# Kernel tuning notes

Measured on AMD Instinct MI355X. Metric: run time of the kernel, lower is better.

Reference implementation:

```python
import jax, jax.numpy as jnp
import numpy as np
from jax import lax

HEADS = 8
LN_EPS = 1e-5


def setup_inputs() -> dict:
    key = jax.random.key(0)
    k = jax.random.split(key, 8)
    B, C, H, W, r = 4, 64, 64, 64, 4
    T = H * W
    x = jax.random.normal(k[0], (B, C, H, W), dtype=jnp.float32)
    conv_w = jax.random.normal(k[1], (C, C, r, r), dtype=jnp.float32) * 0.02  # OIHW
    conv_b = jnp.zeros((C,), dtype=jnp.float32)
    ln_g = jnp.ones((C,), dtype=jnp.float32)
    ln_b = jnp.zeros((C,), dtype=jnp.float32)
    Wqkv = jax.random.normal(k[2], (C, 3 * C), dtype=jnp.float32) * 0.02  # to_qvk (no bias)
    W0 = jax.random.normal(k[3], (C, C), dtype=jnp.float32) * 0.02  # output proj (no bias)
    E = jax.random.normal(k[4], (T, T // 4), dtype=jnp.float32)  # Linformer proj (randn in torch fwd)
    return {"x": x, "conv_w": conv_w, "conv_b": conv_b, "ln_g": ln_g,
            "ln_b": ln_b, "Wqkv": Wqkv, "W0": W0, "E": E}


def _layernorm2d(y, g, b):
    # LayerNorm over channel dim of NCHW (torch: permute to NHWC, LN last dim)
    yt = y.transpose(0, 2, 3, 1)  # b h w c
    mu = yt.mean(-1, keepdims=True)
    var = ((yt - mu) ** 2).mean(-1, keepdims=True)
    yt = (yt - mu) * lax.rsqrt(var + LN_EPS) * g + b
    return yt.transpose(0, 3, 1, 2)


def reference(x, conv_w, conv_b, ln_g, ln_b, Wqkv, W0, E):
    B, C, H, W = x.shape
    T = H * W
    dh = C // HEADS
    r = conv_w.shape[-1]

    # reducer: conv(stride=r) + LayerNorm2d. NOTE: faithful to the torch module,
    # this result is computed but NEVER used by the output (dead code in source).
    red = lax.conv_general_dilated(x, conv_w, (r, r), 'VALID',
                                   dimension_numbers=('NCHW', 'OIHW', 'NCHW'))
    red = red + conv_b[None, :, None, None]
    _red = _layernorm2d(red, ln_g, ln_b)  # unused, matches source

    # tokens from full-resolution x: b c h w -> b (h w) c
    xf = x.reshape(B, C, T).transpose(0, 2, 1)  # [B,T,C]
    qkv = xf @ Wqkv  # [B,T,3C]
    # rearrange 'b t (d k h)' with k=3, h=HEADS -> composite order (d, k, h)
    qkv = qkv.reshape(B, T, dh, 3, HEADS)
    q = qkv[:, :, :, 0, :].transpose(0, 3, 1, 2)  # [B,h,T,d]
    kk = qkv[:, :, :, 1, :].transpose(0, 3, 1, 2)
    v = qkv[:, :, :, 2, :].transpose(0, 3, 1, 2)

    # Linformer low-rank projection of V and K: [B,h,T,d] x [T,k] -> [B,h,k,d]
    v = jnp.einsum('bhjd,jk->bhkd', v, E)
    kk = jnp.einsum('bhjd,jk->bhkd', kk, E)

    scale = dh ** -0.5
    scores = jnp.einsum('bhid,bhjd->bhij', q, kk) * scale  # [B,h,T,k]
    attn = jax.nn.softmax(scores, axis=-1)
    out = jnp.einsum('bhij,bhjd->bhid', attn, v)  # [B,h,T,d]

    out = out.transpose(0, 2, 1, 3).reshape(B, T, C)  # b h i d -> b i (h d)
    out = out @ W0  # [B,T,C]
    return out.transpose(0, 2, 1).reshape(B, C, H, W)
```

## Files before the change

### kernel.cpp

```cpp
#include <hip/hip_runtime.h>

#define T_DIM 4096
#define KD    1024
#define SCALE 0.35355339059327373f

typedef __attribute__((ext_vector_type(8))) short bf16x8;
typedef __attribute__((ext_vector_type(4))) short bf16x4;
typedef __attribute__((ext_vector_type(4))) float f32x4;

__device__ inline unsigned short f2bf(float f) {
  unsigned u = __float_as_uint(f);
  unsigned r = u + 0x7fffu + ((u >> 16) & 1u);
  return (unsigned short)(r >> 16);
}

__device__ inline unsigned cvt_pk_bf16(float a, float b) {
  unsigned ua = __float_as_uint(a); ua += 0x7fffu + ((ua >> 16) & 1u);
  unsigned ub = __float_as_uint(b); ub += 0x7fffu + ((ub >> 16) & 1u);
  return (ua >> 16) | (ub & 0xffff0000u);
}

__device__ inline unsigned pk_trunc(float a, float b) {
  return (__float_as_uint(a) >> 16) | (__float_as_uint(b) & 0xffff0000u);
}

__device__ inline bf16x4 mk4(unsigned lo, unsigned hi) {
  union { unsigned u[2]; bf16x4 v; } x; x.u[0] = lo; x.u[1] = hi; return x.v;
}

__device__ inline bf16x8 mk8(unsigned a, unsigned b, unsigned c, unsigned d) {
  union { unsigned u[4]; bf16x8 v; } x;
  x.u[0] = a; x.u[1] = b; x.u[2] = c; x.u[3] = d; return x.v;
}

__device__ inline f32x4 mfma16(bf16x4 a, bf16x4 b, f32x4 c) {
  bf16x8 a8 = {}, b8 = {};
  a8[0] = a[0]; a8[1] = a[1]; a8[2] = a[2]; a8[3] = a[3];
  b8[0] = b[0]; b8[1] = b[1]; b8[2] = b[2]; b8[3] = b[3];
  return __builtin_amdgcn_mfma_f32_16x16x32_bf16(a8, b8, c, 0, 0, 0);
}

__global__ __launch_bounds__(256) void k_front(const float* __restrict__ x,
                                               const float* __restrict__ E,
                                               const float* __restrict__ Wqkv,
                                               float* __restrict__ partial,
                                               float* __restrict__ Q,
                                               float* __restrict__ out) {
  const int bid = blockIdx.x;
  const int tid = threadIdx.x;

  ((float4*)out)[(size_t)bid * 256 + tid] = make_float4(0.f, 0.f, 0.f, 0.f);

  if (bid < 512) {
    const int kb = bid & 7;
    const int b  = (bid >> 3) & 3;
    const int s  = bid >> 5;
    const int k0 = kb * 128;
    const int lane = tid & 63;
    const int w = tid >> 6;
    const int li = lane & 15, lg = lane >> 4;

    f32x4 acc[4][2] = {};
#pragma unroll 2
    for (int tb = 0; tb < 8; ++tb) {
      const int tbase = s * 256 + tb * 32 + lg * 8;
      bf16x8 bq[2];
#pragma unroll
      for (int nt = 0; nt < 2; ++nt) {
        const int kcol = k0 + w * 32 + nt * 16 + li;
        float bv[8];
#pragma unroll
        for (int j = 0; j < 8; ++j)
          bv[j] = E[(size_t)(tbase + j) * KD + kcol];
        bq[nt] = mk8(cvt_pk_bf16(bv[0], bv[1]), cvt_pk_bf16(bv[2], bv[3]),
                     cvt_pk_bf16(bv[4], bv[5]), cvt_pk_bf16(bv[6], bv[7]));
      }
#pragma unroll
      for (int mt = 0; mt < 4; ++mt) {
        const float* ap = x + ((size_t)b * 64 + mt * 16 + li) * T_DIM + tbase;
        float4 a0 = *(const float4*)(ap);
        float4 a1 = *(const float4*)(ap + 4);
        bf16x8 af8 = mk8(cvt_pk_bf16(a0.x, a0.y), cvt_pk_bf16(a0.z, a0.w),
                         cvt_pk_bf16(a1.x, a1.y), cvt_pk_bf16(a1.z, a1.w));
        acc[mt][0] = __builtin_amdgcn_mfma_f32_16x16x32_bf16(af8, bq[0], acc[mt][0], 0, 0, 0);
        acc[mt][1] = __builtin_amdgcn_mfma_f32_16x16x32_bf16(af8, bq[1], acc[mt][1], 0, 0, 0);
      }
    }
    float* pb = partial + ((size_t)s * 4 + b) * (64 * KD);
#pragma unroll
    for (int mt = 0; mt < 4; ++mt)
#pragma unroll
      for (int nt = 0; nt < 2; ++nt) {
        const int row = mt * 16 + lg * 4;
        const int col = k0 + w * 32 + nt * 16 + li;
#pragma unroll
        for (int reg = 0; reg < 4; ++reg)
          pb[(size_t)(row + reg) * KD + col] = acc[mt][nt][reg];
      }
  } else {
    const int idx = bid - 512;
    const int g  = idx & 7;
    const int tt = (idx >> 3) & 15;
    const int b  = idx >> 7;
    const int t  = tt * 256 + tid;
    const int col0 = g * 24;

    float acc[8];
#pragma unroll
    for (int j = 0; j < 8; ++j) acc[j] = 0.f;
    const float* xb = x + (size_t)b * 64 * T_DIM + t;
#pragma unroll 4
    for (int c = 0; c < 64; ++c) {
      float xv = xb[(size_t)c * T_DIM];
      const float* wr = Wqkv + c * 192 + col0;
#pragma unroll
      for (int h = 0; h < 8; ++h) acc[h] += xv * wr[h];
    }
#pragma unroll
    for (int h = 0; h < 8; ++h)
      Q[(((size_t)(b * 8 + h)) * 8 + g) * T_DIM + t] = acc[h];
  }
}

__global__ __launch_bounds__(256) void k_xkv(const float* __restrict__ partial,
                                             const float* __restrict__ Wqkv,
                                             uint2* __restrict__ Kg,
                                             unsigned short* __restrict__ Vg) {
  __shared__ unsigned short XPs[64 * 72];
  const int kb = blockIdx.x;
  const int h  = blockIdx.y;
  const int b  = blockIdx.z;
  const int tid = threadIdx.x;

  {
    const int kk = tid & 63;
    const int cg = tid >> 6;
#pragma unroll
    for (int u = 0; u < 16; ++u) {
      const int c = cg * 16 + u;
      const size_t src = (size_t)c * KD + kb * 64 + kk;
      float a = 0.f;
#pragma unroll
      for (int s = 0; s < 16; ++s)
        a += partial[((size_t)s * 4 + b) * (64 * KD) + src];
      XPs[c * 72 + kk] = f2bf(a);
    }
  }
  __syncthreads();

  const int klocal = tid & 63;
  const int sel    = (tid >> 6) & 1;
  const int dg     = tid >> 7;
  const int k      = kb * 64 + klocal;

  float acc[4];
#pragma unroll
  for (int d = 0; d < 4; ++d) acc[d] = 0.f;
#pragma unroll 4
  for (int c = 0; c < 64; ++c) {
    float xv = __uint_as_float((unsigned)XPs[c * 72 + klocal] << 16);
    const float* wr = Wqkv + c * 192 + (sel + 1) * 8 + h;
#pragma unroll
    for (int d = 0; d < 4; ++d) acc[d] += xv * wr[(dg * 4 + d) * 24];
  }

  const int bh = b * 8 + h;
  if (sel == 0) {
    uint2* kg = Kg + (size_t)bh * 2048;
    kg[dg * 1024 + k] = make_uint2(cvt_pk_bf16(acc[0] * SCALE, acc[1] * SCALE),
                                   cvt_pk_bf16(acc[2] * SCALE, acc[3] * SCALE));
  } else {
#pragma unroll
    for (int d = 0; d < 4; ++d)
      Vg[(size_t)(bh * 8 + dg * 4 + d) * KD + k] = f2bf(acc[d]);
  }
}

#define VT_PITCH 1032
__global__ __launch_bounds__(256) void k_attn(const float* __restrict__ Q,
                                              const uint2* __restrict__ Kg,
                                              const unsigned short* __restrict__ Vg,
                                              const float* __restrict__ W0,
                                              float* __restrict__ out) {
  __shared__ __attribute__((aligned(16))) unsigned short Kt[2 * 1024 * 4];
  __shared__ unsigned short Vt[9 * VT_PITCH];
  __shared__ float W0s[512];
  const int bh = blockIdx.x;
  const int tid = threadIdx.x;
  const int b = bh >> 3, h = bh & 7;

  const uint2* kg = Kg + (size_t)bh * 2048;
  uint2* kt2 = (uint2*)Kt;
#pragma unroll
  for (int it = 0; it < 8; ++it)
    kt2[it * 256 + tid] = kg[it * 256 + tid];
  const unsigned* vg = (const unsigned*)(Vg + (size_t)bh * 8192);
#pragma unroll
  for (int dd = 0; dd < 8; ++dd) {
#pragma unroll
    for (int it = 0; it < 2; ++it) {
      const int j2 = it * 256 + tid;
      *(unsigned*)(Vt + dd * VT_PITCH + j2 * 2) = vg[dd * 512 + j2];
    }
  }
#pragma unroll
  for (int it = 0; it < 2; ++it)
    *(unsigned*)(Vt + 8 * VT_PITCH + (it * 256 + tid) * 2) = 0x3F803F80u;
  W0s[tid]       = W0[h * 512 + tid];
  W0s[tid + 256] = W0[h * 512 + tid + 256];
  __syncthreads();

  const int lane = tid & 63, w = tid >> 6;
  const int li = lane & 15, lg = lane >> 4;
  const int i0w = blockIdx.y * 128 + w * 32;

  bf16x4 qf[2] = {bf16x4{}, bf16x4{}};
  if (lane < 32) {
#pragma unroll
    for (int it2 = 0; it2 < 2; ++it2) {
      const float* qp = Q + ((size_t)bh * 8 + lg * 4) * T_DIM + i0w + it2 * 16 + li;
      qf[it2] = mk4(cvt_pk_bf16(qp[0], qp[T_DIM]),
                    cvt_pk_bf16(qp[2 * T_DIM], qp[3 * T_DIM]));
    }
  }

  f32x4 accO[2] = {f32x4{0.f, 0.f, 0.f, 0.f}, f32x4{0.f, 0.f, 0.f, 0.f}};
#pragma unroll 2
  for (int jt = 0; jt < 1024; jt += 16) {
    bf16x4 kf = {};
    if (lane < 32) kf = *(const bf16x4*)(&Kt[(size_t)(lg * 1024 + jt + li) * 4]);
    bf16x4 vf = {};
    if (li < 9) vf = *(const bf16x4*)(&Vt[li * VT_PITCH + jt + lg * 4]);
#pragma unroll
    for (int it2 = 0; it2 < 2; ++it2) {
      f32x4 st = mfma16(kf, qf[it2], f32x4{0.f, 0.f, 0.f, 0.f});
      f32x4 p;
      p[0] = __expf(st[0]); p[1] = __expf(st[1]);
      p[2] = __expf(st[2]); p[3] = __expf(st[3]);
      bf16x4 pf = mk4(pk_trunc(p[0], p[1]), pk_trunc(p[2], p[3]));
      accO[it2] = mfma16(vf, pf, accO[it2]);
    }
  }

  __syncthreads();
  float* OwW = (float*)Kt + w * 256;

#pragma unroll
  for (int it2 = 0; it2 < 2; ++it2) {
    float l = __shfl(accO[it2][0], 32 + li);
    float inv = 1.0f / l;
    if (lane < 32) {
      float4 o = make_float4(accO[it2][0] * inv, accO[it2][1] * inv,
                             accO[it2][2] * inv, accO[it2][3] * inv);
      *(float4*)(OwW + (it2 * 16 + li) * 8 + lg * 4) = o;
    }
  }

  const int tok = lane & 31, ch = lane >> 5;
  float ov[8];
#pragma unroll
  for (int d = 0; d < 8; ++d) ov[d] = OwW[tok * 8 + d];
#pragma unroll 4
  for (int j = 0; j < 32; ++j) {
    const int c = ch * 32 + j;
    float a = 0.f;
#pragma unroll
    for (int d = 0; d < 8; ++d) a += ov[d] * W0s[d * 64 + c];
    atomicAdd(out + ((size_t)b * 64 + c) * T_DIM + i0w + tok, a);
  }
}

extern "C" void kernel_launch(void* const* d_in, const int* in_sizes, int n_in,
                              void* d_out, int out_size, void* d_ws, size_t ws_size,
                              hipStream_t stream) {
  const float* x    = (const float*)d_in[0];
  const float* Wqkv = (const float*)d_in[5];
  const float* W0   = (const float*)d_in[6];
  const float* E    = (const float*)d_in[7];
  float* out = (float*)d_out;

  float* Q           = (float*)d_ws;
  float* partial     = Q + 1048576;
  uint2* Kg          = (uint2*)(partial + 4194304);
  unsigned short* Vg = (unsigned short*)(Kg + 65536);

  k_front <<<dim3(1024),     256, 0, stream>>>(x, E, Wqkv, partial, Q, out);
  k_xkv   <<<dim3(16, 8, 4), 256, 0, stream>>>(partial, Wqkv, Kg, Vg);
  k_attn  <<<dim3(32, 32),   256, 0, stream>>>(Q, Kg, Vg, W0, out);
}
```

Baseline: 149.3 us.

## Switch attention to 32x32x16 MFMA with exp2, permlane swaps and halved split-K

The attention inner loop now uses 32x32x16 bf16 MFMA over 32 keys per step instead of padded 16x16x32 calls that carried only 4-wide operands. Scores are pre-scaled by log2(e) so native exp2 can be used, hardware bf16 packing is used, and permlane32 swaps rearrange P into the B operand layout. K is stored interleaved so each lane loads 8 bf16 with one read. The front E-projection GEMM now uses 8 partial splits of 512 tokens instead of 16, which shrinks the partial buffer and the reduction in k_xkv, and k_xkv keeps the reduced values in fp32 shared memory. Risks are lane-layout mistakes in the permuted P fragment and a lower occupancy bound from launch_bounds(256,4).

Result: slower. 157.7 us (+5.6%).

```diff
diff --git a/kernel.cpp b/kernel.cpp
--- a/kernel.cpp
+++ b/kernel.cpp
@@ -2,11 +2,14 @@
 
 #define T_DIM 4096
 #define KD    1024
-#define SCALE 0.35355339059327373f
+#define SCALE2 (0.35355339059327373f * 1.4426950408889634f)
+#define VT_PITCH 1032
+
+extern "C" __device__ float __ocml_native_exp2_f32(float);
 
 typedef __attribute__((ext_vector_type(8))) short bf16x8;
-typedef __attribute__((ext_vector_type(4))) short bf16x4;
 typedef __attribute__((ext_vector_type(4))) float f32x4;
+typedef __attribute__((ext_vector_type(16))) float f32x16;
 
 __device__ inline unsigned short f2bf(float f) {
   unsigned u = __float_as_uint(f);
@@ -20,24 +23,9 @@
   return (ua >> 16) | (ub & 0xffff0000u);
 }
 
-__device__ inline unsigned pk_trunc(float a, float b) {
-  return (__float_as_uint(a) >> 16) | (__float_as_uint(b) & 0xffff0000u);
-}
-
-__device__ inline bf16x4 mk4(unsigned lo, unsigned hi) {
-  union { unsigned u[2]; bf16x4 v; } x; x.u[0] = lo; x.u[1] = hi; return x.v;
-}
-
 __device__ inline bf16x8 mk8(unsigned a, unsigned b, unsigned c, unsigned d) {
   union { unsigned u[4]; bf16x8 v; } x;
   x.u[0] = a; x.u[1] = b; x.u[2] = c; x.u[3] = d; return x.v;
-}
-
-__device__ inline f32x4 mfma16(bf16x4 a, bf16x4 b, f32x4 c) {
-  bf16x8 a8 = {}, b8 = {};
-  a8[0] = a[0]; a8[1] = a[1]; a8[2] = a[2]; a8[3] = a[3];
-  b8[0] = b[0]; b8[1] = b[1]; b8[2] = b[2]; b8[3] = b[3];
-  return __builtin_amdgcn_mfma_f32_16x16x32_bf16(a8, b8, c, 0, 0, 0);
 }
 
 __global__ __launch_bounds__(256) void k_front(const float* __restrict__ x,
@@ -52,29 +40,24 @@
   ((float4*)out)[(size_t)bid * 256 + tid] = make_float4(0.f, 0.f, 0.f, 0.f);
 
   if (bid < 512) {
-    const int kb = bid & 7;
-    const int b  = (bid >> 3) & 3;
-    const int s  = bid >> 5;
-    const int k0 = kb * 128;
+    const int kb = bid & 15;
+    const int b  = (bid >> 4) & 3;
+    const int s  = bid >> 6;
     const int lane = tid & 63;
     const int w = tid >> 6;
     const int li = lane & 15, lg = lane >> 4;
-
-    f32x4 acc[4][2] = {};
+    const int kcol = kb * 64 + w * 16 + li;
+
+    f32x4 acc[4] = {};
 #pragma unroll 2
-    for (int tb = 0; tb < 8; ++tb) {
-      const int tbase = s * 256 + tb * 32 + lg * 8;
-      bf16x8 bq[2];
-#pragma unroll
-      for (int nt = 0; nt < 2; ++nt) {
-        const int kcol = k0 + w * 32 + nt * 16 + li;
-        float bv[8];
-#pragma unroll
-        for (int j = 0; j < 8; ++j)
-          bv[j] = E[(size_t)(tbase + j) * KD + kcol];
-        bq[nt] = mk8(cvt_pk_bf16(bv[0], bv[1]), cvt_pk_bf16(bv[2], bv[3]),
-                     cvt_pk_bf16(bv[4], bv[5]), cvt_pk_bf16(bv[6], bv[7]));
-      }
+    for (int tb = 0; tb < 16; ++tb) {
+      const int tbase = s * 512 + tb * 32 + lg * 8;
+      float bv[8];
+#pragma unroll
+      for (int j = 0; j < 8; ++j)
+        bv[j] = E[(size_t)(tbase + j) * KD + kcol];
+      bf16x8 bq = mk8(cvt_pk_bf16(bv[0], bv[1]), cvt_pk_bf16(bv[2], bv[3]),
+                      cvt_pk_bf16(bv[4], bv[5]), cvt_pk_bf16(bv[6], bv[7]));
 #pragma unroll
       for (int mt = 0; mt < 4; ++mt) {
         const float* ap = x + ((size_t)b * 64 + mt * 16 + li) * T_DIM + tbase;
@@ -82,21 +65,17 @@
         float4 a1 = *(const float4*)(ap + 4);
         bf16x8 af8 = mk8(cvt_pk_bf16(a0.x, a0.y), cvt_pk_bf16(a0.z, a0.w),
                          cvt_pk_bf16(a1.x, a1.y), cvt_pk_bf16(a1.z, a1.w));
-        acc[mt][0] = __builtin_amdgcn_mfma_f32_16x16x32_bf16(af8, bq[0], acc[mt][0], 0, 0, 0);
-        acc[mt][1] = __builtin_amdgcn_mfma_f32_16x16x32_bf16(af8, bq[1], acc[mt][1], 0, 0, 0);
+        acc[mt] = __builtin_amdgcn_mfma_f32_16x16x32_bf16(af8, bq, acc[mt], 0, 0, 0);
       }
     }
     float* pb = partial + ((size_t)s * 4 + b) * (64 * KD);
 #pragma unroll
-    for (int mt = 0; mt < 4; ++mt)
-#pragma unroll
-      for (int nt = 0; nt < 2; ++nt) {
-        const int row = mt * 16 + lg * 4;
-        const int col = k0 + w * 32 + nt * 16 + li;
-#pragma unroll
-        for (int reg = 0; reg < 4; ++reg)
-          pb[(size_t)(row + reg) * KD + col] = acc[mt][nt][reg];
-      }
+    for (int mt = 0; mt < 4; ++mt) {
+      const int row = mt * 16 + lg * 4;
+#pragma unroll
+      for (int reg = 0; reg < 4; ++reg)
+        pb[(size_t)(row + reg) * KD + kcol] = acc[mt][reg];
+    }
   } else {
     const int idx = bid - 512;
     const int g  = idx & 7;
@@ -126,7 +105,7 @@
                                              const float* __restrict__ Wqkv,
                                              uint2* __restrict__ Kg,
                                              unsigned short* __restrict__ Vg) {
-  __shared__ unsigned short XPs[64 * 72];
+  __shared__ float XPs[64 * 64];
   const int kb = blockIdx.x;
   const int h  = blockIdx.y;
   const int b  = blockIdx.z;
@@ -135,15 +114,15 @@
   {
     const int kk = tid & 63;
     const int cg = tid >> 6;
-#pragma unroll
+#pragma unroll 4
     for (int u = 0; u < 16; ++u) {
       const int c = cg * 16 + u;
       const size_t src = (size_t)c * KD + kb * 64 + kk;
       float a = 0.f;
 #pragma unroll
-      for (int s = 0; s < 16; ++s)
+      for (int s = 0; s < 8; ++s)
         a += partial[((size_t)s * 4 + b) * (64 * KD) + src];
-      XPs[c * 72 + kk] = f2bf(a);
+      XPs[c * 64 + kk] = a;
     }
   }
   __syncthreads();
@@ -156,9 +135,9 @@
   float acc[4];
 #pragma unroll
   for (int d = 0; d < 4; ++d) acc[d] = 0.f;
-#pragma unroll 4
+#pragma unroll 8
   for (int c = 0; c < 64; ++c) {
-    float xv = __uint_as_float((unsigned)XPs[c * 72 + klocal] << 16);
+    float xv = XPs[c * 64 + klocal];
     const float* wr = Wqkv + c * 192 + (sel + 1) * 8 + h;
 #pragma unroll
     for (int d = 0; d < 4; ++d) acc[d] += xv * wr[(dg * 4 + d) * 24];
@@ -167,8 +146,8 @@
   const int bh = b * 8 + h;
   if (sel == 0) {
     uint2* kg = Kg + (size_t)bh * 2048;
-    kg[dg * 1024 + k] = make_uint2(cvt_pk_bf16(acc[0] * SCALE, acc[1] * SCALE),
-                                   cvt_pk_bf16(acc[2] * SCALE, acc[3] * SCALE));
+    kg[k * 2 + dg] = make_uint2(cvt_pk_bf16(acc[0] * SCALE2, acc[1] * SCALE2),
+                                cvt_pk_bf16(acc[2] * SCALE2, acc[3] * SCALE2));
   } else {
 #pragma unroll
     for (int d = 0; d < 4; ++d)
@@ -176,24 +155,23 @@
   }
 }
 
-#define VT_PITCH 1032
-__global__ __launch_bounds__(256) void k_attn(const float* __restrict__ Q,
+__global__ __launch_bounds__(256, 4) void k_attn(const float* __restrict__ Q,
                                               const uint2* __restrict__ Kg,
                                               const unsigned short* __restrict__ Vg,
                                               const float* __restrict__ W0,
                                               float* __restrict__ out) {
-  __shared__ __attribute__((aligned(16))) unsigned short Kt[2 * 1024 * 4];
+  __shared__ __attribute__((aligned(16))) unsigned short Kt[1024 * 8];
   __shared__ unsigned short Vt[9 * VT_PITCH];
   __shared__ float W0s[512];
   const int bh = blockIdx.x;
   const int tid = threadIdx.x;
   const int b = bh >> 3, h = bh & 7;
 
-  const uint2* kg = Kg + (size_t)bh * 2048;
-  uint2* kt2 = (uint2*)Kt;
-#pragma unroll
-  for (int it = 0; it < 8; ++it)
-    kt2[it * 256 + tid] = kg[it * 256 + tid];
+  const uint4* kg4 = (const uint4*)(Kg + (size_t)bh * 2048);
+  uint4* kt4 = (uint4*)Kt;
+#pragma unroll
+  for (int it = 0; it < 4; ++it)
+    kt4[it * 256 + tid] = kg4[it * 256 + tid];
   const unsigned* vg = (const unsigned*)(Vg + (size_t)bh * 8192);
 #pragma unroll
   for (int dd = 0; dd < 8; ++dd) {
@@ -211,52 +189,71 @@
   __syncthreads();
 
   const int lane = tid & 63, w = tid >> 6;
-  const int li = lane & 15, lg = lane >> 4;
+  const int icol = lane & 31, half = lane >> 5;
   const int i0w = blockIdx.y * 128 + w * 32;
 
-  bf16x4 qf[2] = {bf16x4{}, bf16x4{}};
+  bf16x8 qf8 = {};
   if (lane < 32) {
-#pragma unroll
-    for (int it2 = 0; it2 < 2; ++it2) {
-      const float* qp = Q + ((size_t)bh * 8 + lg * 4) * T_DIM + i0w + it2 * 16 + li;
-      qf[it2] = mk4(cvt_pk_bf16(qp[0], qp[T_DIM]),
-                    cvt_pk_bf16(qp[2 * T_DIM], qp[3 * T_DIM]));
-    }
-  }
-
-  f32x4 accO[2] = {f32x4{0.f, 0.f, 0.f, 0.f}, f32x4{0.f, 0.f, 0.f, 0.f}};
-#pragma unroll 2
-  for (int jt = 0; jt < 1024; jt += 16) {
-    bf16x4 kf = {};
-    if (lane < 32) kf = *(const bf16x4*)(&Kt[(size_t)(lg * 1024 + jt + li) * 4]);
-    bf16x4 vf = {};
-    if (li < 9) vf = *(const bf16x4*)(&Vt[li * VT_PITCH + jt + lg * 4]);
-#pragma unroll
-    for (int it2 = 0; it2 < 2; ++it2) {
-      f32x4 st = mfma16(kf, qf[it2], f32x4{0.f, 0.f, 0.f, 0.f});
-      f32x4 p;
-      p[0] = __expf(st[0]); p[1] = __expf(st[1]);
-      p[2] = __expf(st[2]); p[3] = __expf(st[3]);
-      bf16x4 pf = mk4(pk_trunc(p[0], p[1]), pk_trunc(p[2], p[3]));
-      accO[it2] = mfma16(vf, pf, accO[it2]);
-    }
+    const float* qp = Q + (size_t)bh * 8 * T_DIM + i0w + icol;
+    float q0 = qp[0],          q1 = qp[T_DIM],     q2 = qp[2 * T_DIM];
+    float q3 = qp[3 * T_DIM],  q4 = qp[4 * T_DIM], q5 = qp[5 * T_DIM];
+    float q6 = qp[6 * T_DIM],  q7 = qp[7 * T_DIM];
+    qf8 = mk8(cvt_pk_bf16(q0, q1), cvt_pk_bf16(q2, q3),
+              cvt_pk_bf16(q4, q5), cvt_pk_bf16(q6, q7));
+  }
+
+  f32x16 accO = {};
+  for (int jt = 0; jt < 1024; jt += 32) {
+    bf16x8 kf8 = {};
+    if (lane < 32) kf8 = *(const bf16x8*)(&Kt[(jt + lane) * 8]);
+    f32x16 z = {};
+    f32x16 st = __builtin_amdgcn_mfma_f32_32x32x16_bf16(kf8, qf8, z, 0, 0, 0);
+
+    unsigned e0, e1, e2, e3, e4, e5, e6, e7;
+    {
+      float p0  = __ocml_native_exp2_f32(st[0]),  p1  = __ocml_native_exp2_f32(st[1]);
+      float p2  = __ocml_native_exp2_f32(st[2]),  p3  = __ocml_native_exp2_f32(st[3]);
+      float p4  = __ocml_native_exp2_f32(st[4]),  p5  = __ocml_native_exp2_f32(st[5]);
+      float p6  = __ocml_native_exp2_f32(st[6]),  p7  = __ocml_native_exp2_f32(st[7]);
+      float p8  = __ocml_native_exp2_f32(st[8]),  p9  = __ocml_native_exp2_f32(st[9]);
+      float p10 = __ocml_native_exp2_f32(st[10]), p11 = __ocml_native_exp2_f32(st[11]);
+      float p12 = __ocml_native_exp2_f32(st[12]), p13 = __ocml_native_exp2_f32(st[13]);
+      float p14 = __ocml_native_exp2_f32(st[14]), p15 = __ocml_native_exp2_f32(st[15]);
+      asm("v_cvt_pk_bf16_f32 %0, %1, %2" : "=v"(e0) : "v"(p0),  "v"(p1));
+      asm("v_cvt_pk_bf16_f32 %0, %1, %2" : "=v"(e1) : "v"(p2),  "v"(p3));
+      asm("v_cvt_pk_bf16_f32 %0, %1, %2" : "=v"(e2) : "v"(p4),  "v"(p5));
+      asm("v_cvt_pk_bf16_f32 %0, %1, %2" : "=v"(e3) : "v"(p6),  "v"(p7));
+      asm("v_cvt_pk_bf16_f32 %0, %1, %2" : "=v"(e4) : "v"(p8),  "v"(p9));
+      asm("v_cvt_pk_bf16_f32 %0, %1, %2" : "=v"(e5) : "v"(p10), "v"(p11));
+      asm("v_cvt_pk_bf16_f32 %0, %1, %2" : "=v"(e6) : "v"(p12), "v"(p13));
+      asm("v_cvt_pk_bf16_f32 %0, %1, %2" : "=v"(e7) : "v"(p14), "v"(p15));
+    }
+    asm("v_permlane32_swap_b32 %0, %1" : "+v"(e0), "+v"(e2));
+    asm("v_permlane32_swap_b32 %0, %1" : "+v"(e1), "+v"(e3));
+    asm("v_permlane32_swap_b32 %0, %1" : "+v"(e4), "+v"(e6));
+    asm("v_permlane32_swap_b32 %0, %1" : "+v"(e5), "+v"(e7));
+
+    bf16x8 va0 = {}, va1 = {};
+    if (icol < 9) {
+      const unsigned short* vp = Vt + icol * VT_PITCH + jt + half * 8;
+      va0 = *(const bf16x8*)(vp);
+      va1 = *(const bf16x8*)(vp + 16);
+    }
+    accO = __builtin_amdgcn_mfma_f32_32x32x16_bf16(va0, mk8(e0, e1, e2, e3), accO, 0, 0, 0);
+    accO = __builtin_amdgcn_mfma_f32_32x32x16_bf16(va1, mk8(e4, e5, e6, e7), accO, 0, 0, 0);
   }
 
   __syncthreads();
   float* OwW = (float*)Kt + w * 256;
 
-#pragma unroll
-  for (int it2 = 0; it2 < 2; ++it2) {
-    float l = __shfl(accO[it2][0], 32 + li);
-    float inv = 1.0f / l;
-    if (lane < 32) {
-      float4 o = make_float4(accO[it2][0] * inv, accO[it2][1] * inv,
-                             accO[it2][2] * inv, accO[it2][3] * inv);
-      *(float4*)(OwW + (it2 * 16 + li) * 8 + lg * 4) = o;
-    }
-  }
-
-  const int tok = lane & 31, ch = lane >> 5;
+  {
+    float inv = 1.0f / __shfl(accO[4], icol);
+    float4 o = make_float4(accO[0] * inv, accO[1] * inv,
+                           accO[2] * inv, accO[3] * inv);
+    *(float4*)(OwW + icol * 8 + half * 4) = o;
+  }
+
+  const int tok = icol, ch = half;
   float ov[8];
 #pragma unroll
   for (int d = 0; d < 8; ++d) ov[d] = OwW[tok * 8 + d];
@@ -281,7 +278,7 @@
 
   float* Q           = (float*)d_ws;
   float* partial     = Q + 1048576;
-  uint2* Kg          = (uint2*)(partial + 4194304);
+  uint2* Kg          = (uint2*)(partial + 2097152);
   unsigned short* Vg = (unsigned short*)(Kg + 65536);
 
   k_front <<<dim3(1024),     256, 0, stream>>>(x, E, Wqkv, partial, Q, out);
```
